# Kernel tuning notes

Hardware: AMD Instinct MI355X
Metric: run time of the kernel (lower is better)

## Reference

```python
import jax, jax.numpy as jnp
import numpy as np

B, N, D = 4, 256, 128
HID = 128
IN_DIM = 4 * D + 4  # h_i, h_j, |h_i-h_j|, h_i*h_j + 2 base + 2 completion feats


def setup_inputs() -> dict:
    key = jax.random.key(0)
    k1, k2, k3, k4, k5, k6, k7 = jax.random.split(key, 7)
    node_latents = jax.random.normal(k1, (B, N, D), dtype=jnp.float32)
    base_edge_logits = jax.random.normal(k2, (B, N, N), dtype=jnp.float32)
    completion_logits = jax.random.normal(k3, (B, N, N), dtype=jnp.float32)
    # MLP params (build_mlp: Linear(in,hid) -> ReLU -> Linear(hid,1) for num_layers=2)
    s1 = 1.0 / np.sqrt(IN_DIM)
    s2 = 1.0 / np.sqrt(HID)
    W1 = jax.random.uniform(k4, (IN_DIM, HID), minval=-s1, maxval=s1, dtype=jnp.float32)
    b1 = jax.random.uniform(k5, (HID,), minval=-s1, maxval=s1, dtype=jnp.float32)
    W2 = jax.random.uniform(k6, (HID, 1), minval=-s2, maxval=s2, dtype=jnp.float32)
    b2 = jax.random.uniform(k7, (1,), minval=-s2, maxval=s2, dtype=jnp.float32)
    return {"node_latents": node_latents, "base_edge_logits": base_edge_logits,
            "completion_logits": completion_logits, "W1": W1, "b1": b1, "W2": W2, "b2": b2}


def reference(node_latents, base_edge_logits, completion_logits, W1, b1, W2, b2):
    bsz, num_nodes, hidden_dim = node_latents.shape
    h_i = jnp.broadcast_to(node_latents[:, :, None, :], (bsz, num_nodes, num_nodes, hidden_dim))
    h_j = jnp.broadcast_to(node_latents[:, None, :, :], (bsz, num_nodes, num_nodes, hidden_dim))
    base = jnp.clip(base_edge_logits, -20.0, 20.0)
    comp = jnp.clip(completion_logits, -20.0, 20.0)
    pair_feat = jnp.concatenate([
        h_i, h_j, jnp.abs(h_i - h_j), h_i * h_j,
        base[..., None], jax.nn.sigmoid(base)[..., None],
        comp[..., None], jax.nn.sigmoid(comp)[..., None],
    ], axis=-1)  # [B, N, N, IN_DIM]
    hdn = jax.nn.relu(jnp.einsum('bijf,fh->bijh', pair_feat, W1) + b1)
    logits = (jnp.einsum('bijh,ho->bijo', hdn, W2) + b2)[..., 0]  # [B, N, N]
    logits = 0.5 * (logits + jnp.swapaxes(logits, 1, 2))
    diag = jnp.eye(num_nodes, dtype=bool)[None]
    return jnp.where(diag, jnp.float32(-1e9), logits)
```

## Files before the change

### kernel.cpp

```cpp
#include <hip/hip_runtime.h>
#include <cstdint>


typedef float f32x4 __attribute__((ext_vector_type(4)));

#define INV256 0.00390625f

__device__ __forceinline__ uint32_t pk4(float a, float b, float c, float d) {
  uint32_t u = __builtin_amdgcn_cvt_pk_fp8_f32(a, b, 0, false);
  u = __builtin_amdgcn_cvt_pk_fp8_f32(c, d, u, true);
  return u;
}
__device__ __forceinline__ long mk64(uint32_t lo, uint32_t hi) {
  return (long)((((unsigned long long)hi) << 32) | lo);
}

__global__ __launch_bounds__(128) void pre_k(const float* __restrict__ node,
                                             const float* __restrict__ W1,
                                             const float* __restrict__ b1,
                                             float* __restrict__ PiB,
                                             float* __restrict__ Pjf,
                                             uint32_t* __restrict__ W1f8) {
  int bid = blockIdx.x;
  int tid = threadIdx.x;
  if (bid < 32) {
    int ks = bid >> 2, nip = (bid >> 1) & 1, wn = bid & 1;
    int lane = tid & 63, nilow = tid >> 6;
    int quad = lane >> 4, col = lane & 15;
    int h = wn * 64 + (nip * 2 + nilow) * 16 + col;
    int k0 = ks * 32 + quad * 8;
    float w[8];
#pragma unroll
    for (int t = 0; t < 8; ++t) w[t] = W1[(256 + k0 + t) * 128 + h] * 256.0f;
    uint2 u;
    u.x = pk4(w[0], w[1], w[2], w[3]);
    u.y = pk4(w[4], w[5], w[6], w[7]);
    reinterpret_cast<uint2*>(W1f8)[(bid * 64 + lane) * 2 + nilow] = u;
  } else {
    __shared__ float sN[128];
    int row = bid - 32;
    int h = tid;
    sN[h] = node[row * 128 + h];
    __syncthreads();
    float ai = 0.f, aj = 0.f;
#pragma unroll 8
    for (int d = 0; d < 128; ++d) {
      float v = sN[d];
      ai = fmaf(v, W1[d * 128 + h], ai);
      aj = fmaf(v, W1[(128 + d) * 128 + h], aj);
    }
    PiB[row * 128 + h] = ai + b1[h];
    Pjf[row * 128 + h] = aj;
  }
}

__global__ __launch_bounds__(256, 3) void main_k(
    const float* __restrict__ node, const float* __restrict__ baseL,
    const float* __restrict__ compL, const float* __restrict__ W1,
    const float* __restrict__ W2, const float* __restrict__ b2,
    const uint32_t* __restrict__ W1f8, const float* __restrict__ PiB,
    const float* __restrict__ Pjf, float* __restrict__ out) {
  __shared__ __align__(16) char smem[16640 + 32768];
  __shared__ float sScalF[64][4];
  __shared__ float sScalM[64][4];
  char* sF = smem;
  char* sB = smem + 16640;
  float* sNode = reinterpret_cast<float*>(sB);

  const int tid = threadIdx.x;
  const int bx = blockIdx.x;
  const int b = bx / 528;
  const int t = bx - b * 528;
  int tI = (int)((65.0f - sqrtf(4225.0f - 8.0f * (float)t)) * 0.5f);
  tI = (tI < 0) ? 0 : (tI > 31 ? 31 : tI);
  while (((65 * tI - tI * tI) >> 1) > t) --tI;
  while (tI < 31 && ((65 * (tI + 1) - (tI + 1) * (tI + 1)) >> 1) <= t) ++tI;
  const int tJ = tI + (t - ((65 * tI - tI * tI) >> 1));
  const int I0 = tI * 8, J0 = tJ * 8;
  const int rowB = b * 256;

  const int lane = tid & 63;
  const int wave = tid >> 6;
  const int wm = wave >> 1, wn = wave & 1;
  const int col = lane & 15, quad = lane >> 4;

  uint4 g[8];
#pragma unroll
  for (int it = 0; it < 8; ++it)
    g[it] = reinterpret_cast<const uint4*>(W1f8)[it * 256 + tid];

#pragma unroll
  for (int it = 0; it < 2; ++it) {
    int idx = it * 256 + tid;
    int row = idx >> 5, d4 = idx & 31;
    int gr = rowB + ((row < 8) ? (I0 + row) : (J0 + row - 8));
    reinterpret_cast<float4*>(sNode)[idx] =
        reinterpret_cast<const float4*>(node + (size_t)gr * 128)[d4];
  }

  if (tid < 128) {
    int p = tid & 63;
    int mir = tid >> 6;
    int iN = I0 + (p >> 3), jN = J0 + (p & 7);
    int rr = mir ? jN : iN, cc = mir ? iN : jN;
    float bl = fminf(fmaxf(baseL[(size_t)(rowB + rr) * 256 + cc], -20.f), 20.f);
    float cl = fminf(fmaxf(compL[(size_t)(rowB + rr) * 256 + cc], -20.f), 20.f);
    float* dst = mir ? sScalM[p] : sScalF[p];
    dst[0] = bl;
    dst[1] = 1.f / (1.f + __expf(-bl));
    dst[2] = cl;
    dst[3] = 1.f / (1.f + __expf(-cl));
  }

  float cW2[4], cB0[4], cB1[4], cB2[4], cB3[4];
#pragma unroll
  for (int ni = 0; ni < 4; ++ni) {
    int h = wn * 64 + ni * 16 + col;
    cW2[ni] = W2[h];
    cB0[ni] = W1[512 * 128 + h];
    cB1[ni] = W1[513 * 128 + h];
    cB2[ni] = W1[514 * 128 + h];
    cB3[ni] = W1[515 * 128 + h];
  }
  const float b2v = b2[0];

  float piI[2][4], pjI[2][4], piJ[4][4], pjJ[4][4];
#pragma unroll
  for (int mi = 0; mi < 2; ++mi) {
    int gi = rowB + I0 + wm * 4 + mi * 2 + (quad >> 1);
#pragma unroll
    for (int ni = 0; ni < 4; ++ni) {
      int h = wn * 64 + ni * 16 + col;
      piI[mi][ni] = PiB[(size_t)gi * 128 + h];
      pjI[mi][ni] = Pjf[(size_t)gi * 128 + h];
    }
  }
#pragma unroll
  for (int r = 0; r < 4; ++r) {
    int gj = rowB + J0 + (quad & 1) * 4 + r;
#pragma unroll
    for (int ni = 0; ni < 4; ++ni) {
      int h = wn * 64 + ni * 16 + col;
      piJ[r][ni] = PiB[(size_t)gj * 128 + h];
      pjJ[r][ni] = Pjf[(size_t)gj * 128 + h];
    }
  }
  __syncthreads();

  {
    const int d4 = tid & 31;
    const int rr = tid >> 5;
    const int ks1 = d4 >> 3, qj = (d4 >> 1) & 3, kb = (d4 & 1) * 4;
    const float4 hj = reinterpret_cast<const float4*>(sNode + (8 + rr) * 128)[d4];
#pragma unroll
    for (int pass = 0; pass < 8; ++pass) {
      const float4 hi = reinterpret_cast<const float4*>(sNode + pass * 128)[d4];
      uint32_t du = pk4(fabsf(hi.x - hj.x), fabsf(hi.y - hj.y),
                        fabsf(hi.z - hj.z), fabsf(hi.w - hj.w));
      uint32_t pu = pk4(hi.x * hj.x, hi.y * hj.y, hi.z * hj.z, hi.w * hj.w);
      int p = pass * 8 + rr;
      int colj = p & 15, m16 = p >> 4;
      int off = (m16 >> 1) * 1024 + (qj * 16 + colj) * 16 + (m16 & 1) * 8 + kb;
      *reinterpret_cast<uint32_t*>(sF + ks1 * 2080 + off) = du;
      *reinterpret_cast<uint32_t*>(sF + (4 + ks1) * 2080 + off) = pu;
    }
  }
  __syncthreads();
#pragma unroll
  for (int it = 0; it < 8; ++it)
    reinterpret_cast<uint4*>(sB)[it * 256 + tid] = g[it];
  __syncthreads();

  f32x4 acc[2][4] = {};
#pragma unroll
  for (int ks = 0; ks < 8; ++ks) {
    uint4 b01 = *reinterpret_cast<const uint4*>(sB + ((ks * 2 + 0) * 2 + wn) * 1024 + lane * 16);
    uint4 b23 = *reinterpret_cast<const uint4*>(sB + ((ks * 2 + 1) * 2 + wn) * 1024 + lane * 16);
    uint4 aa = *reinterpret_cast<const uint4*>(sF + ks * 2080 + wm * 1024 + lane * 16);
    long a0 = mk64(aa.x, aa.y), a1 = mk64(aa.z, aa.w);
    long bb0 = mk64(b01.x, b01.y), bb1 = mk64(b01.z, b01.w);
    long bb2 = mk64(b23.x, b23.y), bb3 = mk64(b23.z, b23.w);
    acc[0][0] = __builtin_amdgcn_mfma_f32_16x16x32_fp8_fp8(a0, bb0, acc[0][0], 0, 0, 0);
    acc[0][1] = __builtin_amdgcn_mfma_f32_16x16x32_fp8_fp8(a0, bb1, acc[0][1], 0, 0, 0);
    acc[0][2] = __builtin_amdgcn_mfma_f32_16x16x32_fp8_fp8(a0, bb2, acc[0][2], 0, 0, 0);
    acc[0][3] = __builtin_amdgcn_mfma_f32_16x16x32_fp8_fp8(a0, bb3, acc[0][3], 0, 0, 0);
    acc[1][0] = __builtin_amdgcn_mfma_f32_16x16x32_fp8_fp8(a1, bb0, acc[1][0], 0, 0, 0);
    acc[1][1] = __builtin_amdgcn_mfma_f32_16x16x32_fp8_fp8(a1, bb1, acc[1][1], 0, 0, 0);
    acc[1][2] = __builtin_amdgcn_mfma_f32_16x16x32_fp8_fp8(a1, bb2, acc[1][2], 0, 0, 0);
    acc[1][3] = __builtin_amdgcn_mfma_f32_16x16x32_fp8_fp8(a1, bb3, acc[1][3], 0, 0, 0);
  }

  __syncthreads();
  float(*sPF)[33] = reinterpret_cast<float(*)[33]>(smem);
  float(*sPM)[33] = reinterpret_cast<float(*)[33]>(smem + 16640);

#pragma unroll
  for (int mi = 0; mi < 2; ++mi) {
#pragma unroll
    for (int r = 0; r < 4; ++r) {
      int p = wm * 32 + mi * 16 + quad * 4 + r;
      float f0 = sScalF[p][0], f1 = sScalF[p][1], f2 = sScalF[p][2], f3 = sScalF[p][3];
      float m0 = sScalM[p][0], m1 = sScalM[p][1], m2 = sScalM[p][2], m3 = sScalM[p][3];
      float vf = 0.f, vm = 0.f;
#pragma unroll
      for (int ni = 0; ni < 4; ++ni) {
        float gv = acc[mi][ni][r] * INV256;
        float pf = (gv + piI[mi][ni]) + pjJ[r][ni];
        pf = fmaf(f0, cB0[ni], pf);
        pf = fmaf(f1, cB1[ni], pf);
        pf = fmaf(f2, cB2[ni], pf);
        pf = fmaf(f3, cB3[ni], pf);
        float pm = (gv + piJ[r][ni]) + pjI[mi][ni];
        pm = fmaf(m0, cB0[ni], pm);
        pm = fmaf(m1, cB1[ni], pm);
        pm = fmaf(m2, cB2[ni], pm);
        pm = fmaf(m3, cB3[ni], pm);
        vf = fmaf(fmaxf(pf, 0.f), cW2[ni], vf);
        vm = fmaf(fmaxf(pm, 0.f), cW2[ni], vm);
      }
      sPF[p][wn * 16 + col] = vf;
      sPM[p][wn * 16 + col] = vm;
    }
  }
  __syncthreads();
  if (tid < 64) {
    int p = tid;
    float sumF = 0.f, sumM = 0.f;
#pragma unroll
    for (int c = 0; c < 32; ++c) {
      sumF += sPF[p][c];
      sumM += sPM[p][c];
    }
    float val = 0.5f * (sumF + sumM) + b2v;
    int iN = I0 + (p >> 3), jN = J0 + (p & 7);
    if (iN == jN) {
      out[(size_t)(rowB + iN) * 256 + jN] = -1e9f;
    } else {
      out[(size_t)(rowB + iN) * 256 + jN] = val;
      out[(size_t)(rowB + jN) * 256 + iN] = val;
    }
  }
}

extern "C" void kernel_launch(void* const* d_in, const int* in_sizes, int n_in,
                              void* d_out, int out_size, void* d_ws, size_t ws_size,
                              hipStream_t stream) {
  const float* node = (const float*)d_in[0];
  const float* baseL = (const float*)d_in[1];
  const float* compL = (const float*)d_in[2];
  const float* W1 = (const float*)d_in[3];
  const float* b1 = (const float*)d_in[4];
  const float* W2 = (const float*)d_in[5];
  const float* b2 = (const float*)d_in[6];
  float* out = (float*)d_out;

  char* ws = (char*)d_ws;
  float* PiB = (float*)(ws);
  float* Pjf = (float*)(ws + (512 << 10));
  uint32_t* W1f8 = (uint32_t*)(ws + (1024 << 10));

  pre_k<<<1056, 128, 0, stream>>>(node, W1, b1, PiB, Pjf, W1f8);
  main_k<<<2112, 256, 0, stream>>>(node, baseL, compL, W1, W2, b2, W1f8, PiB, Pjf, out);
}
```

Measured before the change: 108.0 us.

## Stream W1 fragments from global and stage projections in LDS as bf16

Removes the 32KB LDS staging of the FP8 W1 tile and loads MFMA B fragments straight from global or L2 inside the k-loop. Per-node projection vectors PiB/Pjf are no longer held in 48 registers per thread; they are stored once into shared memory as truncated bf16 and read back in the epilogue. Launch bounds are raised to 4 blocks per SM to exploit the lower LDS and register footprint. The risks are global-load latency inside the MFMA loop and the precision loss from truncating the projections to bf16.

```diff
diff --git a/kernel.cpp b/kernel.cpp
--- a/kernel.cpp
+++ b/kernel.cpp
@@ -10,6 +10,15 @@
   uint32_t u = __builtin_amdgcn_cvt_pk_fp8_f32(a, b, 0, false);
   u = __builtin_amdgcn_cvt_pk_fp8_f32(c, d, u, true);
   return u;
+}
+__device__ __forceinline__ uint32_t pkbf2(float lo, float hi) {
+  uint32_t l = __builtin_bit_cast(uint32_t, lo);
+  uint32_t h = __builtin_bit_cast(uint32_t, hi);
+  return (l >> 16) | (h & 0xffff0000u);
+}
+__device__ __forceinline__ float bf2f(unsigned short u) {
+  uint32_t x = ((uint32_t)u) << 16;
+  return __builtin_bit_cast(float, x);
 }
 __device__ __forceinline__ long mk64(uint32_t lo, uint32_t hi) {
   return (long)((((unsigned long long)hi) << 32) | lo);
@@ -54,18 +63,18 @@
   }
 }
 
-__global__ __launch_bounds__(256, 3) void main_k(
+__global__ __launch_bounds__(256, 4) void main_k(
     const float* __restrict__ node, const float* __restrict__ baseL,
     const float* __restrict__ compL, const float* __restrict__ W1,
     const float* __restrict__ W2, const float* __restrict__ b2,
     const uint32_t* __restrict__ W1f8, const float* __restrict__ PiB,
     const float* __restrict__ Pjf, float* __restrict__ out) {
-  __shared__ __align__(16) char smem[16640 + 32768];
+  __shared__ __align__(16) char smem[25088];
+  __shared__ unsigned short sPP[32 * 136];
   __shared__ float sScalF[64][4];
   __shared__ float sScalM[64][4];
   char* sF = smem;
-  char* sB = smem + 16640;
-  float* sNode = reinterpret_cast<float*>(sB);
+  float* sNode = reinterpret_cast<float*>(smem + 16640);
 
   const int tid = threadIdx.x;
   const int bx = blockIdx.x;
@@ -84,11 +93,6 @@
   const int wm = wave >> 1, wn = wave & 1;
   const int col = lane & 15, quad = lane >> 4;
 
-  uint4 g[8];
-#pragma unroll
-  for (int it = 0; it < 8; ++it)
-    g[it] = reinterpret_cast<const uint4*>(W1f8)[it * 256 + tid];
-
 #pragma unroll
   for (int it = 0; it < 2; ++it) {
     int idx = it * 256 + tid;
@@ -96,6 +100,20 @@
     int gr = rowB + ((row < 8) ? (I0 + row) : (J0 + row - 8));
     reinterpret_cast<float4*>(sNode)[idx] =
         reinterpret_cast<const float4*>(node + (size_t)gr * 128)[d4];
+  }
+
+#pragma unroll
+  for (int it = 0; it < 4; ++it) {
+    int idx = it * 256 + tid;
+    int row = idx >> 5, d4 = idx & 31;
+    int rr = row & 15;
+    const float* src = (row < 16) ? PiB : Pjf;
+    int gr = rowB + ((rr < 8) ? (I0 + rr) : (J0 + rr - 8));
+    float4 v = reinterpret_cast<const float4*>(src + (size_t)gr * 128)[d4];
+    uint2 u;
+    u.x = pkbf2(v.x, v.y);
+    u.y = pkbf2(v.z, v.w);
+    *reinterpret_cast<uint2*>(&sPP[row * 136 + d4 * 4]) = u;
   }
 
   if (tid < 128) {
@@ -123,28 +141,6 @@
     cB3[ni] = W1[515 * 128 + h];
   }
   const float b2v = b2[0];
-
-  float piI[2][4], pjI[2][4], piJ[4][4], pjJ[4][4];
-#pragma unroll
-  for (int mi = 0; mi < 2; ++mi) {
-    int gi = rowB + I0 + wm * 4 + mi * 2 + (quad >> 1);
-#pragma unroll
-    for (int ni = 0; ni < 4; ++ni) {
-      int h = wn * 64 + ni * 16 + col;
-      piI[mi][ni] = PiB[(size_t)gi * 128 + h];
-      pjI[mi][ni] = Pjf[(size_t)gi * 128 + h];
-    }
-  }
-#pragma unroll
-  for (int r = 0; r < 4; ++r) {
-    int gj = rowB + J0 + (quad & 1) * 4 + r;
-#pragma unroll
-    for (int ni = 0; ni < 4; ++ni) {
-      int h = wn * 64 + ni * 16 + col;
-      piJ[r][ni] = PiB[(size_t)gj * 128 + h];
-      pjJ[r][ni] = Pjf[(size_t)gj * 128 + h];
-    }
-  }
   __syncthreads();
 
   {
@@ -166,16 +162,13 @@
     }
   }
   __syncthreads();
-#pragma unroll
-  for (int it = 0; it < 8; ++it)
-    reinterpret_cast<uint4*>(sB)[it * 256 + tid] = g[it];
-  __syncthreads();
-
+
+  const uint4* Bg = reinterpret_cast<const uint4*>(W1f8);
   f32x4 acc[2][4] = {};
 #pragma unroll
   for (int ks = 0; ks < 8; ++ks) {
-    uint4 b01 = *reinterpret_cast<const uint4*>(sB + ((ks * 2 + 0) * 2 + wn) * 1024 + lane * 16);
-    uint4 b23 = *reinterpret_cast<const uint4*>(sB + ((ks * 2 + 1) * 2 + wn) * 1024 + lane * 16);
+    uint4 b01 = Bg[((ks * 2 + 0) * 2 + wn) * 64 + lane];
+    uint4 b23 = Bg[((ks * 2 + 1) * 2 + wn) * 64 + lane];
     uint4 aa = *reinterpret_cast<const uint4*>(sF + ks * 2080 + wm * 1024 + lane * 16);
     long a0 = mk64(aa.x, aa.y), a1 = mk64(aa.z, aa.w);
     long bb0 = mk64(b01.x, b01.y), bb1 = mk64(b01.z, b01.w);
@@ -199,18 +192,25 @@
 #pragma unroll
     for (int r = 0; r < 4; ++r) {
       int p = wm * 32 + mi * 16 + quad * 4 + r;
+      int iRow = wm * 4 + mi * 2 + (quad >> 1);
+      int jRow = (quad & 1) * 4 + r;
       float f0 = sScalF[p][0], f1 = sScalF[p][1], f2 = sScalF[p][2], f3 = sScalF[p][3];
       float m0 = sScalM[p][0], m1 = sScalM[p][1], m2 = sScalM[p][2], m3 = sScalM[p][3];
       float vf = 0.f, vm = 0.f;
 #pragma unroll
       for (int ni = 0; ni < 4; ++ni) {
+        int h = wn * 64 + ni * 16 + col;
+        float piI = bf2f(sPP[(0 + iRow) * 136 + h]);
+        float piJ = bf2f(sPP[(8 + jRow) * 136 + h]);
+        float pjI = bf2f(sPP[(16 + iRow) * 136 + h]);
+        float pjJ = bf2f(sPP[(24 + jRow) * 136 + h]);
         float gv = acc[mi][ni][r] * INV256;
-        float pf = (gv + piI[mi][ni]) + pjJ[r][ni];
+        float pf = (gv + piI) + pjJ;
         pf = fmaf(f0, cB0[ni], pf);
         pf = fmaf(f1, cB1[ni], pf);
         pf = fmaf(f2, cB2[ni], pf);
         pf = fmaf(f3, cB3[ni], pf);
-        float pm = (gv + piJ[r][ni]) + pjI[mi][ni];
+        float pm = (gv + piJ) + pjI;
         pm = fmaf(m0, cB0[ni], pm);
         pm = fmaf(m1, cB1[ni], pm);
         pm = fmaf(m2, cB2[ni], pm);
```

New measurement: 98.47 us. -8.9%, faster.

## Enlarge pair tiles to 16x16 and keep W1 fp8 fragments in registers

Applied to the files above, without the earlier changes.

Each block now covers a 16x16 tile of upper-triangular node pairs instead of 8x8, processed in two halves of 8 rows, so the grid shrinks from 2112 to 544 blocks. Each wave keeps its slice of the fp8 W1 fragments in registers rather than staging them through shared memory. Per-node projections and clipped scalar features are packed as bf16 pairs in shared memory. The cross-wave reduction uses lane shuffles. This amortizes the W1 and node loads over four times as many pairs and cuts shared-memory traffic, at the cost of fewer blocks, lower occupancy (launch bounds 2) and bf16 rounding of the projection terms.

```diff
diff --git a/kernel.cpp b/kernel.cpp
--- a/kernel.cpp
+++ b/kernel.cpp
@@ -5,11 +5,30 @@
 typedef float f32x4 __attribute__((ext_vector_type(4)));
 
 #define INV256 0.00390625f
+
+#define SF_OFF 0
+#define SNODE_OFF 33024
+#define SPP_OFF 49408
+#define SCAL_OFF 66304
+#define SPF_OFF 70400
+#define SPM_OFF 72448
+#define SMEM_TOTAL 74496
 
 __device__ __forceinline__ uint32_t pk4(float a, float b, float c, float d) {
   uint32_t u = __builtin_amdgcn_cvt_pk_fp8_f32(a, b, 0, false);
   u = __builtin_amdgcn_cvt_pk_fp8_f32(c, d, u, true);
   return u;
+}
+__device__ __forceinline__ uint32_t pkbf2(float lo, float hi) {
+  uint32_t l = __builtin_bit_cast(uint32_t, lo);
+  uint32_t h = __builtin_bit_cast(uint32_t, hi);
+  return (l >> 16) | (h & 0xffff0000u);
+}
+__device__ __forceinline__ float ulo(uint32_t u) {
+  return __builtin_bit_cast(float, u << 16);
+}
+__device__ __forceinline__ float uhi(uint32_t u) {
+  return __builtin_bit_cast(float, u & 0xffff0000u);
 }
 __device__ __forceinline__ long mk64(uint32_t lo, uint32_t hi) {
   return (long)((((unsigned long long)hi) << 32) | lo);
@@ -54,191 +73,207 @@
   }
 }
 
-__global__ __launch_bounds__(256, 3) void main_k(
+__global__ __launch_bounds__(256, 2) void main_k(
     const float* __restrict__ node, const float* __restrict__ baseL,
     const float* __restrict__ compL, const float* __restrict__ W1,
     const float* __restrict__ W2, const float* __restrict__ b2,
     const uint32_t* __restrict__ W1f8, const float* __restrict__ PiB,
     const float* __restrict__ Pjf, float* __restrict__ out) {
-  __shared__ __align__(16) char smem[16640 + 32768];
-  __shared__ float sScalF[64][4];
-  __shared__ float sScalM[64][4];
+  __shared__ __align__(16) char smem[SMEM_TOTAL];
   char* sF = smem;
-  char* sB = smem + 16640;
-  float* sNode = reinterpret_cast<float*>(sB);
+  float* sNode = reinterpret_cast<float*>(smem + SNODE_OFF);
+  uint32_t* sPP = reinterpret_cast<uint32_t*>(smem + SPP_OFF);
+  uint4* sScal = reinterpret_cast<uint4*>(smem + SCAL_OFF);
+  float* sPF = reinterpret_cast<float*>(smem + SPF_OFF);
+  float* sPM = reinterpret_cast<float*>(smem + SPM_OFF);
 
   const int tid = threadIdx.x;
   const int bx = blockIdx.x;
-  const int b = bx / 528;
-  const int t = bx - b * 528;
-  int tI = (int)((65.0f - sqrtf(4225.0f - 8.0f * (float)t)) * 0.5f);
-  tI = (tI < 0) ? 0 : (tI > 31 ? 31 : tI);
-  while (((65 * tI - tI * tI) >> 1) > t) --tI;
-  while (tI < 31 && ((65 * (tI + 1) - (tI + 1) * (tI + 1)) >> 1) <= t) ++tI;
-  const int tJ = tI + (t - ((65 * tI - tI * tI) >> 1));
-  const int I0 = tI * 8, J0 = tJ * 8;
+  const int b = bx / 136;
+  const int t = bx - b * 136;
+  int tI = (int)((33.0f - sqrtf(1089.0f - 8.0f * (float)t)) * 0.5f);
+  tI = (tI < 0) ? 0 : (tI > 15 ? 15 : tI);
+  while ((16 * tI - ((tI * (tI - 1)) >> 1)) > t) --tI;
+  while (tI < 15 && (16 * (tI + 1) - (((tI + 1) * tI) >> 1)) <= t) ++tI;
+  const int tJ = tI + (t - (16 * tI - ((tI * (tI - 1)) >> 1)));
+  const int I0 = tI * 16, J0 = tJ * 16;
   const int rowB = b * 256;
 
   const int lane = tid & 63;
-  const int wave = tid >> 6;
-  const int wm = wave >> 1, wn = wave & 1;
+  const int wn2 = tid >> 6;
   const int col = lane & 15, quad = lane >> 4;
 
-  uint4 g[8];
-#pragma unroll
-  for (int it = 0; it < 8; ++it)
-    g[it] = reinterpret_cast<const uint4*>(W1f8)[it * 256 + tid];
-
-#pragma unroll
-  for (int it = 0; it < 2; ++it) {
+  const int uB = ((wn2 & 1) << 1) | (wn2 >> 1);
+  uint4 gB[8];
+#pragma unroll
+  for (int ks = 0; ks < 8; ++ks)
+    gB[ks] = reinterpret_cast<const uint4*>(W1f8)[(ks * 4 + uB) * 64 + lane];
+
+#pragma unroll
+  for (int it = 0; it < 4; ++it) {
     int idx = it * 256 + tid;
     int row = idx >> 5, d4 = idx & 31;
-    int gr = rowB + ((row < 8) ? (I0 + row) : (J0 + row - 8));
-    reinterpret_cast<float4*>(sNode)[idx] =
+    int gr = rowB + ((row < 16) ? (I0 + row) : (J0 + row - 16));
+    reinterpret_cast<float4*>(sNode)[row * 32 + d4] =
         reinterpret_cast<const float4*>(node + (size_t)gr * 128)[d4];
   }
 
-  if (tid < 128) {
-    int p = tid & 63;
-    int mir = tid >> 6;
-    int iN = I0 + (p >> 3), jN = J0 + (p & 7);
-    int rr = mir ? jN : iN, cc = mir ? iN : jN;
-    float bl = fminf(fmaxf(baseL[(size_t)(rowB + rr) * 256 + cc], -20.f), 20.f);
-    float cl = fminf(fmaxf(compL[(size_t)(rowB + rr) * 256 + cc], -20.f), 20.f);
-    float* dst = mir ? sScalM[p] : sScalF[p];
-    dst[0] = bl;
-    dst[1] = 1.f / (1.f + __expf(-bl));
-    dst[2] = cl;
-    dst[3] = 1.f / (1.f + __expf(-cl));
-  }
-
-  float cW2[4], cB0[4], cB1[4], cB2[4], cB3[4];
-#pragma unroll
-  for (int ni = 0; ni < 4; ++ni) {
-    int h = wn * 64 + ni * 16 + col;
-    cW2[ni] = W2[h];
+#pragma unroll
+  for (int it = 0; it < 4; ++it) {
+    int idx = it * 256 + tid;
+    int row = idx >> 5, d4 = idx & 31;
+    int gr = rowB + ((row < 16) ? (I0 + row) : (J0 + row - 16));
+    float4 a = reinterpret_cast<const float4*>(PiB + (size_t)gr * 128)[d4];
+    float4 c = reinterpret_cast<const float4*>(Pjf + (size_t)gr * 128)[d4];
+    uint4 u;
+    u.x = pkbf2(a.x, c.x);
+    u.y = pkbf2(a.y, c.y);
+    u.z = pkbf2(a.z, c.z);
+    u.w = pkbf2(a.w, c.w);
+    *reinterpret_cast<uint4*>(&sPP[row * 132 + d4 * 4]) = u;
+  }
+
+  {
+    int p = tid;
+    int iN = I0 + (p >> 4), jN = J0 + (p & 15);
+    float blf = fminf(fmaxf(baseL[(size_t)(rowB + iN) * 256 + jN], -20.f), 20.f);
+    float clf = fminf(fmaxf(compL[(size_t)(rowB + iN) * 256 + jN], -20.f), 20.f);
+    float blm = fminf(fmaxf(baseL[(size_t)(rowB + jN) * 256 + iN], -20.f), 20.f);
+    float clm = fminf(fmaxf(compL[(size_t)(rowB + jN) * 256 + iN], -20.f), 20.f);
+    uint4 u;
+    u.x = pkbf2(blf, 1.f / (1.f + __expf(-blf)));
+    u.y = pkbf2(clf, 1.f / (1.f + __expf(-clf)));
+    u.z = pkbf2(blm, 1.f / (1.f + __expf(-blm)));
+    u.w = pkbf2(clm, 1.f / (1.f + __expf(-clm)));
+    sScal[p] = u;
+  }
+
+  float cB0[2], cB1[2], cB2[2], cB3[2], cW2[2];
+#pragma unroll
+  for (int ni = 0; ni < 2; ++ni) {
+    int h = (wn2 * 2 + ni) * 16 + col;
     cB0[ni] = W1[512 * 128 + h];
     cB1[ni] = W1[513 * 128 + h];
     cB2[ni] = W1[514 * 128 + h];
     cB3[ni] = W1[515 * 128 + h];
+    cW2[ni] = W2[h];
   }
   const float b2v = b2[0];
-
-  float piI[2][4], pjI[2][4], piJ[4][4], pjJ[4][4];
-#pragma unroll
-  for (int mi = 0; mi < 2; ++mi) {
-    int gi = rowB + I0 + wm * 4 + mi * 2 + (quad >> 1);
-#pragma unroll
-    for (int ni = 0; ni < 4; ++ni) {
-      int h = wn * 64 + ni * 16 + col;
-      piI[mi][ni] = PiB[(size_t)gi * 128 + h];
-      pjI[mi][ni] = Pjf[(size_t)gi * 128 + h];
-    }
-  }
-#pragma unroll
-  for (int r = 0; r < 4; ++r) {
-    int gj = rowB + J0 + (quad & 1) * 4 + r;
-#pragma unroll
-    for (int ni = 0; ni < 4; ++ni) {
-      int h = wn * 64 + ni * 16 + col;
-      piJ[r][ni] = PiB[(size_t)gj * 128 + h];
-      pjJ[r][ni] = Pjf[(size_t)gj * 128 + h];
-    }
-  }
   __syncthreads();
 
-  {
-    const int d4 = tid & 31;
-    const int rr = tid >> 5;
-    const int ks1 = d4 >> 3, qj = (d4 >> 1) & 3, kb = (d4 & 1) * 4;
-    const float4 hj = reinterpret_cast<const float4*>(sNode + (8 + rr) * 128)[d4];
-#pragma unroll
-    for (int pass = 0; pass < 8; ++pass) {
-      const float4 hi = reinterpret_cast<const float4*>(sNode + pass * 128)[d4];
-      uint32_t du = pk4(fabsf(hi.x - hj.x), fabsf(hi.y - hj.y),
-                        fabsf(hi.z - hj.z), fabsf(hi.w - hj.w));
-      uint32_t pu = pk4(hi.x * hj.x, hi.y * hj.y, hi.z * hj.z, hi.w * hj.w);
-      int p = pass * 8 + rr;
-      int colj = p & 15, m16 = p >> 4;
-      int off = (m16 >> 1) * 1024 + (qj * 16 + colj) * 16 + (m16 & 1) * 8 + kb;
-      *reinterpret_cast<uint32_t*>(sF + ks1 * 2080 + off) = du;
-      *reinterpret_cast<uint32_t*>(sF + (4 + ks1) * 2080 + off) = pu;
-    }
-  }
-  __syncthreads();
-#pragma unroll
-  for (int it = 0; it < 8; ++it)
-    reinterpret_cast<uint4*>(sB)[it * 256 + tid] = g[it];
-  __syncthreads();
-
-  f32x4 acc[2][4] = {};
-#pragma unroll
-  for (int ks = 0; ks < 8; ++ks) {
-    uint4 b01 = *reinterpret_cast<const uint4*>(sB + ((ks * 2 + 0) * 2 + wn) * 1024 + lane * 16);
-    uint4 b23 = *reinterpret_cast<const uint4*>(sB + ((ks * 2 + 1) * 2 + wn) * 1024 + lane * 16);
-    uint4 aa = *reinterpret_cast<const uint4*>(sF + ks * 2080 + wm * 1024 + lane * 16);
-    long a0 = mk64(aa.x, aa.y), a1 = mk64(aa.z, aa.w);
-    long bb0 = mk64(b01.x, b01.y), bb1 = mk64(b01.z, b01.w);
-    long bb2 = mk64(b23.x, b23.y), bb3 = mk64(b23.z, b23.w);
-    acc[0][0] = __builtin_amdgcn_mfma_f32_16x16x32_fp8_fp8(a0, bb0, acc[0][0], 0, 0, 0);
-    acc[0][1] = __builtin_amdgcn_mfma_f32_16x16x32_fp8_fp8(a0, bb1, acc[0][1], 0, 0, 0);
-    acc[0][2] = __builtin_amdgcn_mfma_f32_16x16x32_fp8_fp8(a0, bb2, acc[0][2], 0, 0, 0);
-    acc[0][3] = __builtin_amdgcn_mfma_f32_16x16x32_fp8_fp8(a0, bb3, acc[0][3], 0, 0, 0);
-    acc[1][0] = __builtin_amdgcn_mfma_f32_16x16x32_fp8_fp8(a1, bb0, acc[1][0], 0, 0, 0);
-    acc[1][1] = __builtin_amdgcn_mfma_f32_16x16x32_fp8_fp8(a1, bb1, acc[1][1], 0, 0, 0);
-    acc[1][2] = __builtin_amdgcn_mfma_f32_16x16x32_fp8_fp8(a1, bb2, acc[1][2], 0, 0, 0);
-    acc[1][3] = __builtin_amdgcn_mfma_f32_16x16x32_fp8_fp8(a1, bb3, acc[1][3], 0, 0, 0);
-  }
-
-  __syncthreads();
-  float(*sPF)[33] = reinterpret_cast<float(*)[33]>(smem);
-  float(*sPM)[33] = reinterpret_cast<float(*)[33]>(smem + 16640);
-
-#pragma unroll
-  for (int mi = 0; mi < 2; ++mi) {
-#pragma unroll
-    for (int r = 0; r < 4; ++r) {
-      int p = wm * 32 + mi * 16 + quad * 4 + r;
-      float f0 = sScalF[p][0], f1 = sScalF[p][1], f2 = sScalF[p][2], f3 = sScalF[p][3];
-      float m0 = sScalM[p][0], m1 = sScalM[p][1], m2 = sScalM[p][2], m3 = sScalM[p][3];
-      float vf = 0.f, vm = 0.f;
-#pragma unroll
-      for (int ni = 0; ni < 4; ++ni) {
-        float gv = acc[mi][ni][r] * INV256;
-        float pf = (gv + piI[mi][ni]) + pjJ[r][ni];
-        pf = fmaf(f0, cB0[ni], pf);
-        pf = fmaf(f1, cB1[ni], pf);
-        pf = fmaf(f2, cB2[ni], pf);
-        pf = fmaf(f3, cB3[ni], pf);
-        float pm = (gv + piJ[r][ni]) + pjI[mi][ni];
-        pm = fmaf(m0, cB0[ni], pm);
-        pm = fmaf(m1, cB1[ni], pm);
-        pm = fmaf(m2, cB2[ni], pm);
-        pm = fmaf(m3, cB3[ni], pm);
-        vf = fmaf(fmaxf(pf, 0.f), cW2[ni], vf);
-        vm = fmaf(fmaxf(pm, 0.f), cW2[ni], vm);
-      }
-      sPF[p][wn * 16 + col] = vf;
-      sPM[p][wn * 16 + col] = vm;
-    }
-  }
-  __syncthreads();
-  if (tid < 64) {
-    int p = tid;
-    float sumF = 0.f, sumM = 0.f;
-#pragma unroll
-    for (int c = 0; c < 32; ++c) {
-      sumF += sPF[p][c];
-      sumM += sPM[p][c];
-    }
-    float val = 0.5f * (sumF + sumM) + b2v;
-    int iN = I0 + (p >> 3), jN = J0 + (p & 7);
-    if (iN == jN) {
-      out[(size_t)(rowB + iN) * 256 + jN] = -1e9f;
-    } else {
+#pragma unroll 1
+  for (int H = 0; H < 2; ++H) {
+    {
+      const int d4 = tid & 31;
+      const int rr = tid >> 5;
+      const int ks1 = d4 >> 3, qd = (d4 >> 1) & 3, kb = (d4 & 1) * 4;
+#pragma unroll
+      for (int js = 0; js < 2; ++js) {
+        int jj = rr + js * 8;
+        const float4 hj = reinterpret_cast<const float4*>(sNode)[(16 + jj) * 32 + d4];
+        int scol = ((jj + 2 * qd) & 15);
+        uint32_t base = ks1 * 4128 + qd * 128 + scol * 8 + kb;
+#pragma unroll
+        for (int iiL = 0; iiL < 8; ++iiL) {
+          const float4 hi = reinterpret_cast<const float4*>(sNode)[(H * 8 + iiL) * 32 + d4];
+          uint32_t du = pk4(fabsf(hi.x - hj.x), fabsf(hi.y - hj.y),
+                            fabsf(hi.z - hj.z), fabsf(hi.w - hj.w));
+          uint32_t pu = pk4(hi.x * hj.x, hi.y * hj.y, hi.z * hj.z, hi.w * hj.w);
+          uint32_t addr = base + iiL * 512;
+          *reinterpret_cast<uint32_t*>(sF + addr) = du;
+          *reinterpret_cast<uint32_t*>(sF + addr + 4 * 4128) = pu;
+        }
+      }
+    }
+    __syncthreads();
+
+    f32x4 acc[8][2] = {};
+    const int ascol = ((col + 2 * quad) & 15);
+    const char* aBase = sF + quad * 128 + ascol * 8;
+#pragma unroll
+    for (int ks = 0; ks < 8; ++ks) {
+      long bb0 = mk64(gB[ks].x, gB[ks].y);
+      long bb1 = mk64(gB[ks].z, gB[ks].w);
+#pragma unroll
+      for (int mi = 0; mi < 8; ++mi) {
+        uint2 av = *reinterpret_cast<const uint2*>(aBase + ks * 4128 + mi * 512);
+        long aa = mk64(av.x, av.y);
+        acc[mi][0] = __builtin_amdgcn_mfma_f32_16x16x32_fp8_fp8(aa, bb0, acc[mi][0], 0, 0, 0);
+        acc[mi][1] = __builtin_amdgcn_mfma_f32_16x16x32_fp8_fp8(aa, bb1, acc[mi][1], 0, 0, 0);
+      }
+    }
+    __syncthreads();
+
+    uint32_t ppJ[4][2];
+#pragma unroll
+    for (int r = 0; r < 4; ++r)
+#pragma unroll
+      for (int ni = 0; ni < 2; ++ni)
+        ppJ[r][ni] = sPP[(16 + quad * 4 + r) * 132 + (wn2 * 2 + ni) * 16 + col];
+
+#pragma unroll
+    for (int mi = 0; mi < 8; ++mi) {
+      const int iiF = H * 8 + mi;
+      float piI[2], pjI[2];
+#pragma unroll
+      for (int ni = 0; ni < 2; ++ni) {
+        uint32_t u = sPP[iiF * 132 + (wn2 * 2 + ni) * 16 + col];
+        piI[ni] = ulo(u);
+        pjI[ni] = uhi(u);
+      }
+#pragma unroll
+      for (int r = 0; r < 4; ++r) {
+        int p = mi * 16 + quad * 4 + r;
+        uint4 sc = sScal[p];
+        float f0 = ulo(sc.x), f1 = uhi(sc.x), f2 = ulo(sc.y), f3 = uhi(sc.y);
+        float m0 = ulo(sc.z), m1 = uhi(sc.z), m2 = ulo(sc.w), m3 = uhi(sc.w);
+        float vf = 0.f, vm = 0.f;
+#pragma unroll
+        for (int ni = 0; ni < 2; ++ni) {
+          float piJ = ulo(ppJ[r][ni]), pjJ = uhi(ppJ[r][ni]);
+          float gv = acc[mi][ni][r] * INV256;
+          float pf = (gv + piI[ni]) + pjJ;
+          pf = fmaf(f0, cB0[ni], pf);
+          pf = fmaf(f1, cB1[ni], pf);
+          pf = fmaf(f2, cB2[ni], pf);
+          pf = fmaf(f3, cB3[ni], pf);
+          float pm = (gv + piJ) + pjI[ni];
+          pm = fmaf(m0, cB0[ni], pm);
+          pm = fmaf(m1, cB1[ni], pm);
+          pm = fmaf(m2, cB2[ni], pm);
+          pm = fmaf(m3, cB3[ni], pm);
+          vf = fmaf(fmaxf(pf, 0.f), cW2[ni], vf);
+          vm = fmaf(fmaxf(pm, 0.f), cW2[ni], vm);
+        }
+        vf += __shfl_xor(vf, 1);
+        vf += __shfl_xor(vf, 2);
+        vf += __shfl_xor(vf, 4);
+        vf += __shfl_xor(vf, 8);
+        vm += __shfl_xor(vm, 1);
+        vm += __shfl_xor(vm, 2);
+        vm += __shfl_xor(vm, 4);
+        vm += __shfl_xor(vm, 8);
+        if (col == 0) {
+          sPF[p * 4 + wn2] = vf;
+          sPM[p * 4 + wn2] = vm;
+        }
+      }
+    }
+    __syncthreads();
+
+    if (tid < 128) {
+      int p = tid;
+      float4 pf4 = reinterpret_cast<const float4*>(sPF)[p];
+      float4 pm4 = reinterpret_cast<const float4*>(sPM)[p];
+      float val = 0.5f * ((pf4.x + pf4.y + pf4.z + pf4.w) +
+                          (pm4.x + pm4.y + pm4.z + pm4.w)) + b2v;
+      int iN = I0 + H * 8 + (p >> 4);
+      int jN = J0 + (p & 15);
+      if (iN == jN) val = -1e9f;
       out[(size_t)(rowB + iN) * 256 + jN] = val;
       out[(size_t)(rowB + jN) * 256 + iN] = val;
     }
+    __syncthreads();
   }
 }
 
@@ -260,5 +295,5 @@
   uint32_t* W1f8 = (uint32_t*)(ws + (1024 << 10));
 
   pre_k<<<1056, 128, 0, stream>>>(node, W1, b1, PiB, Pjf, W1f8);
-  main_k<<<2112, 256, 0, stream>>>(node, baseL, compL, W1, W2, b2, W1f8, PiB, Pjf, out);
-}
+  main_k<<<544, 256, 0, stream>>>(node, baseL, compL, W1, W2, b2, W1f8, PiB, Pjf, out);
+}
```

Result: slower. 126.5 us (+17.1%).
